# Performance work log

Hardware: AMD Instinct MI355X
Metric: run time of the kernel (lower is better)

Reference implementation:

```python
import jax, jax.numpy as jnp
import numpy as np

B = 16384
FEAT_SIZES = [1000000, 1000000, 500000, 500000, 100000, 100000, 10000, 10000]
EMB_DIM = 50          # min(50, feat_size//2) for all chosen sizes
CONT_IN = 64
D = 8 * EMB_DIM + 64  # 464 = total_embedding_size + 64
H1, H2 = 256, 128     # expert/cross hidden sizes
E, T = 4, 3           # num_experts, num_tasks


def setup_inputs() -> dict:
    key = jax.random.key(0)
    ks = iter(jax.random.split(key, 64))
    s = 0.02
    inp = {}
    inp["discrete_features"] = jax.random.randint(next(ks), (B, 8), 0, 10000)
    inp["continuous_features"] = jax.random.normal(next(ks), (B, CONT_IN), jnp.float32)
    for i, fs in enumerate(FEAT_SIZES):
        inp[f"emb{i}"] = jax.random.normal(next(ks), (fs, EMB_DIM), jnp.float32) * s
    inp["cont_W"] = jax.random.normal(next(ks), (CONT_IN, 64), jnp.float32) * s
    inp["cont_b"] = jnp.zeros((64,), jnp.float32)
    inp["fm_W"] = jax.random.normal(next(ks), (D, 10), jnp.float32) * s
    inp["cW1"] = jax.random.normal(next(ks), (D, H1), jnp.float32) * s
    inp["cb1"] = jnp.zeros((H1,), jnp.float32)
    inp["cW2"] = jax.random.normal(next(ks), (H1, H2), jnp.float32) * s
    inp["cb2"] = jnp.zeros((H2,), jnp.float32)
    inp["coW"] = jax.random.normal(next(ks), (H2, D), jnp.float32) * s
    inp["cob"] = jnp.zeros((D,), jnp.float32)
    inp["expW1"] = jax.random.normal(next(ks), (E, D, H1), jnp.float32) * s
    inp["expb1"] = jnp.zeros((E, H1), jnp.float32)
    inp["expW2"] = jax.random.normal(next(ks), (E, H1, H2), jnp.float32) * s
    inp["expb2"] = jnp.zeros((E, H2), jnp.float32)
    inp["gate_W"] = jax.random.normal(next(ks), (T, D, E), jnp.float32) * s
    inp["gate_b"] = jnp.zeros((T, E), jnp.float32)
    inp["task_W"] = jax.random.normal(next(ks), (T, H2, 1), jnp.float32) * s
    inp["task_b"] = jnp.zeros((T, 1), jnp.float32)
    inp["log_vars"] = jnp.zeros((T,), jnp.float32)
    return inp


def reference(discrete_features, continuous_features,
              emb0, emb1, emb2, emb3, emb4, emb5, emb6, emb7,
              cont_W, cont_b, fm_W, cW1, cb1, cW2, cb2, coW, cob,
              expW1, expb1, expW2, expb2, gate_W, gate_b,
              task_W, task_b, log_vars):
    tables = [emb0, emb1, emb2, emb3, emb4, emb5, emb6, emb7]
    embs = [jnp.take(t, discrete_features[:, i], axis=0) for i, t in enumerate(tables)]
    cont = jax.nn.relu(continuous_features @ cont_W + cont_b)           # [B,64]
    x = jnp.concatenate(embs + [cont], axis=1)                          # [B,D]
    # FM part: x @ fm_embedding.weight -> [B,10], square-of-sum minus sum-of-square
    xe = x @ fm_W
    fm = 0.5 * (jnp.sum(xe, 1, keepdims=True) ** 2
                - jnp.sum(xe ** 2, 1, keepdims=True))                   # [B,1]
    # cross network
    c = jax.nn.relu(x @ cW1 + cb1)
    c = jax.nn.relu(c @ cW2 + cb2)
    co = c @ coW + cob                                                  # [B,D]
    h = x + co + fm                                                     # [B,D] (fm broadcast)
    # experts as batched GEMMs: [B,E,H2]
    e1 = jax.nn.relu(jnp.einsum('bd,edh->beh', h, expW1) + expb1)
    eo = jnp.einsum('beh,eho->beo', e1, expW2) + expb2
    # gates: [B,T,E] softmax over experts
    g = jax.nn.softmax(jnp.einsum('bd,tde->bte', h, gate_W) + gate_b, axis=-1)
    mixed = jnp.einsum('bte,beo->bto', g, eo)                           # [B,T,H2]
    out = jnp.einsum('bto,tok->btk', mixed, task_W) + task_b            # [B,T,1]
    return out[..., 0], log_vars                                        # ([B,3], [3])
```

## Files before the change

### kernel.cpp

```cpp
#include <hip/hip_runtime.h>
#include <stdint.h>

typedef _Float16 f16;
typedef __attribute__((ext_vector_type(8))) _Float16 f16x8;
typedef __attribute__((ext_vector_type(4))) float    f32x4;

constexpr int BROWS = 16384;
constexpr int NTASK = 3;

constexpr int OFF_CW1 = 0;
constexpr int OFF_CW2 = OFF_CW1 + 256 * 480;
constexpr int OFF_COW = OFF_CW2 + 128 * 256;
constexpr int OFF_EW1 = OFF_COW + 512 * 128;
constexpr int OFF_EW2 = OFF_EW1 + 1024 * 480;
constexpr int OFF_FMW = OFF_EW2 + 512 * 256;
constexpr int OFF_GW  = OFF_FMW + 16 * 480;
constexpr int OFF_CTW = OFF_GW  + 16 * 480;
constexpr int PACK_TOTAL = OFF_CTW + 64 * 64;

__global__ __launch_bounds__(256)
void pack_all(const float* __restrict__ cW1, const float* __restrict__ cW2,
              const float* __restrict__ coW, const float* __restrict__ expW1,
              const float* __restrict__ expW2, const float* __restrict__ fmW,
              const float* __restrict__ gateW, const float* __restrict__ contW,
              f16* __restrict__ wp)
{
    const int idx = blockIdx.x * 256 + threadIdx.x;
    if (idx >= PACK_TOTAL) return;
    float v = 0.f;
    if (idx < OFF_CW2) {
        const int l = idx - OFF_CW1, n = l / 480, k = l % 480;
        if (k < 464) v = cW1[k * 256 + n];
    } else if (idx < OFF_COW) {
        const int l = idx - OFF_CW2, n = l / 256, k = l % 256;
        v = cW2[k * 128 + n];
    } else if (idx < OFF_EW1) {
        const int l = idx - OFF_COW, n = l / 128, k = l % 128;
        if (n < 464) v = coW[k * 464 + n];
    } else if (idx < OFF_EW2) {
        const int l = idx - OFF_EW1, n = l / 480, k = l % 480;
        const int e = n >> 8, nn = n & 255;
        if (k < 464) v = expW1[(e * 464 + k) * 256 + nn];
    } else if (idx < OFF_FMW) {
        const int l = idx - OFF_EW2, n = l / 256, k = l % 256;
        const int e = n >> 7, nn = n & 127;
        v = expW2[(e * 256 + k) * 128 + nn];
    } else if (idx < OFF_GW) {
        const int l = idx - OFF_FMW, c = l / 480, k = l % 480;
        if (c < 10 && k < 464) v = fmW[k * 10 + c];
    } else if (idx < OFF_CTW) {
        const int l = idx - OFF_GW, c = l / 480, k = l % 480;
        if (c < 12 && k < 464) {
            const int tt = c >> 2, e = c & 3;
            v = gateW[(tt * 464 + k) * 4 + e];
        }
    } else {
        const int l = idx - OFF_CTW, n = l / 64, k = l % 64;
        v = contW[k * 64 + n];
    }
    wp[idx] = (f16)v;
}

template<int MF, int NF, int KS, int LDA>
__device__ __forceinline__ void wave_gemm(
    const f16* __restrict__ As, int arow0,
    const f16* __restrict__ Bg, int bcol0, int ldb,
    f32x4 (&acc)[MF][NF], int lane)
{
    const int g = lane >> 4, rr = lane & 15;
#pragma unroll
    for (int kb = 0; kb < KS; ++kb) {
        const int ko = kb * 32 + g * 8;
        f16x8 bf[NF];
#pragma unroll
        for (int j = 0; j < NF; ++j)
            bf[j] = *(const f16x8*)(Bg + (long)(bcol0 + j * 16 + rr) * ldb + ko);
#pragma unroll
        for (int i = 0; i < MF; ++i) {
            const f16x8 af = *(const f16x8*)(As + (arow0 + i * 16 + rr) * LDA + ko);
#pragma unroll
            for (int j = 0; j < NF; ++j)
                acc[i][j] = __builtin_amdgcn_mfma_f32_16x16x32_f16(
                    af, bf[j], acc[i][j], 0, 0, 0);
        }
    }
}

__global__ __launch_bounds__(256, 1)
void mmoe_fused(const int* __restrict__ disc, const float* __restrict__ cf,
                const float* __restrict__ e0p, const float* __restrict__ e1p,
                const float* __restrict__ e2p, const float* __restrict__ e3p,
                const float* __restrict__ e4p, const float* __restrict__ e5p,
                const float* __restrict__ e6p, const float* __restrict__ e7p,
                const float* __restrict__ contB, const float* __restrict__ cb1,
                const float* __restrict__ cb2, const float* __restrict__ cob,
                const float* __restrict__ expb1, const float* __restrict__ expb2,
                const float* __restrict__ gateB, const float* __restrict__ taskW,
                const float* __restrict__ taskB, const float* __restrict__ logv,
                const f16* __restrict__ wp, float* __restrict__ out)
{
    __shared__ f16   sh_x [64][488];
    __shared__ f16   sh_c1[64][264];
    __shared__ f16   sh_c2[64][136];
    __shared__ float sh_g [64][12];
    __shared__ float sh_part[4][64][3];
    __shared__ float sh_fm[64];
    __shared__ const float* stabs[8];

    const int t = threadIdx.x;
    const int lane = t & 63, wave = t >> 6;
    const int g = lane >> 4, rr = lane & 15;
    const long r0 = (long)blockIdx.x * 64;

    const f16* cW1p = wp + OFF_CW1;
    const f16* cW2p = wp + OFF_CW2;
    const f16* coWp = wp + OFF_COW;
    const f16* eW1p = wp + OFF_EW1;
    const f16* eW2p = wp + OFF_EW2;
    const f16* fmWp = wp + OFF_FMW;
    const f16* gWp  = wp + OFF_GW;
    const f16* ctWp = wp + OFF_CTW;

    if (t == 0) {
        stabs[0] = e0p; stabs[1] = e1p; stabs[2] = e2p; stabs[3] = e3p;
        stabs[4] = e4p; stabs[5] = e5p; stabs[6] = e6p; stabs[7] = e7p;
    }
    __syncthreads();

    f16* cfp = (f16*)&sh_c2[0][0];
    for (int i = t; i < 64 * 24; i += 256) sh_x[i / 24][464 + i % 24] = (f16)0.f;
    for (int p = t; p < 512; p += 256) {
        const int r = p >> 3, tab = p & 7;
        const long fi = disc[(r0 + r) * 8 + tab];
        const float* src = stabs[tab] + fi * 50;
        f16* dst = &sh_x[r][tab * 50];
#pragma unroll
        for (int q = 0; q < 25; ++q) {
            const float2 v = *(const float2*)(src + q * 2);
            dst[q * 2] = (f16)v.x; dst[q * 2 + 1] = (f16)v.y;
        }
    }
    for (int i = t; i < 64 * 16; i += 256) {
        const int r = i >> 4, q = i & 15;
        const float4 v = *(const float4*)(cf + (r0 + r) * 64 + q * 4);
        f16* dst = cfp + r * 72 + q * 4;
        dst[0] = (f16)v.x; dst[1] = (f16)v.y; dst[2] = (f16)v.z; dst[3] = (f16)v.w;
    }
    __syncthreads();

    {
        f32x4 acc[4][1] = {};
        wave_gemm<4, 1, 2, 72>(cfp, 0, ctWp, wave * 16, 64, acc, lane);
        const int col = wave * 16 + rr;
        const float bv = contB[col];
#pragma unroll
        for (int i = 0; i < 4; ++i)
#pragma unroll
            for (int rx = 0; rx < 4; ++rx)
                sh_x[i * 16 + g * 4 + rx][400 + col] =
                    (f16)fmaxf(acc[i][0][rx] + bv, 0.f);
    }
    __syncthreads();

    {
        f32x4 a[1][1] = {};
        wave_gemm<1, 1, 15, 488>(&sh_x[0][0], wave * 16, fmWp, 0, 480, a, lane);
#pragma unroll
        for (int rx = 0; rx < 4; ++rx) {
            const float v = a[0][0][rx];
            float s = v, ss = v * v;
#pragma unroll
            for (int off = 1; off < 16; off <<= 1) {
                s += __shfl_xor(s, off, 64); ss += __shfl_xor(ss, off, 64);
            }
            if (rr == 0) sh_fm[wave * 16 + g * 4 + rx] = 0.5f * (s * s - ss);
        }
    }
    {
        f32x4 acc[4][4] = {};
        wave_gemm<4, 4, 15, 488>(&sh_x[0][0], 0, cW1p, wave * 64, 480, acc, lane);
#pragma unroll
        for (int j = 0; j < 4; ++j) {
            const int col = wave * 64 + j * 16 + rr;
            const float bv = cb1[col];
#pragma unroll
            for (int i = 0; i < 4; ++i)
#pragma unroll
                for (int rx = 0; rx < 4; ++rx)
                    sh_c1[i * 16 + g * 4 + rx][col] =
                        (f16)fmaxf(acc[i][j][rx] + bv, 0.f);
        }
    }
    __syncthreads();

    {
        f32x4 acc[4][2] = {};
        wave_gemm<4, 2, 8, 264>(&sh_c1[0][0], 0, cW2p, wave * 32, 256, acc, lane);
#pragma unroll
        for (int j = 0; j < 2; ++j) {
            const int col = wave * 32 + j * 16 + rr;
            const float bv = cb2[col];
#pragma unroll
            for (int i = 0; i < 4; ++i)
#pragma unroll
                for (int rx = 0; rx < 4; ++rx)
                    sh_c2[i * 16 + g * 4 + rx][col] =
                        (f16)fmaxf(acc[i][j][rx] + bv, 0.f);
        }
    }
    __syncthreads();

    {
        f32x4 acc[4][8] = {};
        wave_gemm<4, 8, 4, 136>(&sh_c2[0][0], 0, coWp, wave * 128, 128, acc, lane);
#pragma unroll
        for (int j = 0; j < 8; ++j) {
            const int col = wave * 128 + j * 16 + rr;
            if (col < 464) {
                const float bv = cob[col];
#pragma unroll
                for (int i = 0; i < 4; ++i)
#pragma unroll
                    for (int rx = 0; rx < 4; ++rx) {
                        const int row = i * 16 + g * 4 + rx;
                        const float v = acc[i][j][rx] + bv +
                                        (float)sh_x[row][col] + sh_fm[row];
                        sh_x[row][col] = (f16)v;
                    }
            }
        }
    }
    __syncthreads();

    {
        f32x4 a[1][1] = {};
        wave_gemm<1, 1, 15, 488>(&sh_x[0][0], wave * 16, gWp, 0, 480, a, lane);
        const float gb = (rr < 12) ? gateB[rr] : 0.f;
#pragma unroll
        for (int rx = 0; rx < 4; ++rx) {
            const float v = a[0][0][rx] + gb;
            float m = fmaxf(v, __shfl_xor(v, 1, 64));
            m = fmaxf(m, __shfl_xor(m, 2, 64));
            const float p = __expf(v - m);
            float s = p + __shfl_xor(p, 1, 64);
            s += __shfl_xor(s, 2, 64);
            if (rr < 12) sh_g[wave * 16 + g * 4 + rx][rr] = p / s;
        }
    }
    __syncthreads();

    float tw[3][2];
#pragma unroll
    for (int tt = 0; tt < 3; ++tt) {
        tw[tt][0] = taskW[tt * 128 + wave * 32 + rr];
        tw[tt][1] = taskW[tt * 128 + wave * 32 + 16 + rr];
    }
    float oacc[4][4][3];
#pragma unroll
    for (int i = 0; i < 4; ++i)
#pragma unroll
        for (int rx = 0; rx < 4; ++rx)
#pragma unroll
            for (int tt = 0; tt < 3; ++tt) oacc[i][rx][tt] = 0.f;

#pragma unroll 1
    for (int e = 0; e < 4; ++e) {
        {
            f32x4 acc[4][4] = {};
            wave_gemm<4, 4, 15, 488>(&sh_x[0][0], 0, eW1p + e * (256 * 480),
                                     wave * 64, 480, acc, lane);
#pragma unroll
            for (int j = 0; j < 4; ++j) {
                const int col = wave * 64 + j * 16 + rr;
                const float bv = expb1[e * 256 + col];
#pragma unroll
                for (int i = 0; i < 4; ++i)
#pragma unroll
                    for (int rx = 0; rx < 4; ++rx)
                        sh_c1[i * 16 + g * 4 + rx][col] =
                            (f16)fmaxf(acc[i][j][rx] + bv, 0.f);
            }
        }
        __syncthreads();
        {
            f32x4 acc[4][2] = {};
            wave_gemm<4, 2, 8, 264>(&sh_c1[0][0], 0, eW2p + e * (128 * 256),
                                    wave * 32, 256, acc, lane);
            const float bv0 = expb2[e * 128 + wave * 32 + rr];
            const float bv1 = expb2[e * 128 + wave * 32 + 16 + rr];
#pragma unroll
            for (int i = 0; i < 4; ++i)
#pragma unroll
                for (int rx = 0; rx < 4; ++rx) {
                    const int row = i * 16 + g * 4 + rx;
                    const float v0 = acc[i][0][rx] + bv0;
                    const float v1 = acc[i][1][rx] + bv1;
#pragma unroll
                    for (int tt = 0; tt < 3; ++tt) {
                        float s = v0 * tw[tt][0] + v1 * tw[tt][1];
#pragma unroll
                        for (int off = 1; off < 16; off <<= 1)
                            s += __shfl_xor(s, off, 64);
                        oacc[i][rx][tt] += sh_g[row][tt * 4 + e] * s;
                    }
                }
        }
        __syncthreads();
    }

    if (rr == 0) {
#pragma unroll
        for (int i = 0; i < 4; ++i)
#pragma unroll
            for (int rx = 0; rx < 4; ++rx)
#pragma unroll
                for (int tt = 0; tt < 3; ++tt)
                    sh_part[wave][i * 16 + g * 4 + rx][tt] = oacc[i][rx][tt];
    }
    __syncthreads();
    for (int i = t; i < 64 * 3; i += 256) {
        const int row = i / 3, tt = i - row * 3;
        out[(r0 + row) * 3 + tt] = sh_part[0][row][tt] + sh_part[1][row][tt] +
                                   sh_part[2][row][tt] + sh_part[3][row][tt] +
                                   taskB[tt];
    }
    if (blockIdx.x == 0 && t < NTASK) out[(long)BROWS * 3 + t] = logv[t];
}

extern "C" void kernel_launch(void* const* d_in, const int* in_sizes, int n_in,
                              void* d_out, int out_size, void* d_ws, size_t ws_size,
                              hipStream_t stream)
{
    (void)in_sizes; (void)n_in; (void)out_size; (void)ws_size;

    const int*   disc  = (const int*)  d_in[0];
    const float* cf    = (const float*)d_in[1];
    const float* emb0  = (const float*)d_in[2];
    const float* emb1  = (const float*)d_in[3];
    const float* emb2  = (const float*)d_in[4];
    const float* emb3  = (const float*)d_in[5];
    const float* emb4  = (const float*)d_in[6];
    const float* emb5  = (const float*)d_in[7];
    const float* emb6  = (const float*)d_in[8];
    const float* emb7  = (const float*)d_in[9];
    const float* contW = (const float*)d_in[10];
    const float* contB = (const float*)d_in[11];
    const float* fmW   = (const float*)d_in[12];
    const float* cW1   = (const float*)d_in[13];
    const float* cb1   = (const float*)d_in[14];
    const float* cW2   = (const float*)d_in[15];
    const float* cb2   = (const float*)d_in[16];
    const float* coW   = (const float*)d_in[17];
    const float* cob   = (const float*)d_in[18];
    const float* expW1 = (const float*)d_in[19];
    const float* expb1 = (const float*)d_in[20];
    const float* expW2 = (const float*)d_in[21];
    const float* expb2 = (const float*)d_in[22];
    const float* gateW = (const float*)d_in[23];
    const float* gateB = (const float*)d_in[24];
    const float* taskW = (const float*)d_in[25];
    const float* taskB = (const float*)d_in[26];
    const float* logv  = (const float*)d_in[27];

    f16* wp = (f16*)d_ws;

    pack_all<<<(PACK_TOTAL + 255) / 256, 256, 0, stream>>>(
        cW1, cW2, coW, expW1, expW2, fmW, gateW, contW, wp);

    mmoe_fused<<<BROWS / 64, 256, 0, stream>>>(
        disc, cf, emb0, emb1, emb2, emb3, emb4, emb5, emb6, emb7,
        contB, cb1, cb2, cob, expb1, expb2, gateB, taskW, taskB, logv,
        wp, (float*)d_out);
}
```

Before: 100.7 us.

## Use 512-thread blocks, split GEMM columns across 8 waves, defer task-head reduction

Doubles the workgroup to 8 waves, so each wave computes half as many output columns in every GEMM stage. This cuts per-wave accumulator registers and adds more waves to hide latency. The per-expert shuffle reduction for the task head is replaced by per-lane accumulation, with a single cross-lane reduction at the end. The fm and gate stages now use only 4 of the 8 waves, and A-fragment loads from shared memory are duplicated across more waves.

Measured after the change: 106.5 us. 1.06x slower.

```diff
diff --git a/kernel.cpp b/kernel.cpp
--- a/kernel.cpp
+++ b/kernel.cpp
@@ -86,7 +86,7 @@
     }
 }
 
-__global__ __launch_bounds__(256, 1)
+__global__ __launch_bounds__(512, 1)
 void mmoe_fused(const int* __restrict__ disc, const float* __restrict__ cf,
                 const float* __restrict__ e0p, const float* __restrict__ e1p,
                 const float* __restrict__ e2p, const float* __restrict__ e3p,
@@ -103,7 +103,7 @@
     __shared__ f16   sh_c1[64][264];
     __shared__ f16   sh_c2[64][136];
     __shared__ float sh_g [64][12];
-    __shared__ float sh_part[4][64][3];
+    __shared__ float sh_part[8][64][3];
     __shared__ float sh_fm[64];
     __shared__ const float* stabs[8];
 
@@ -128,9 +128,9 @@
     __syncthreads();
 
     f16* cfp = (f16*)&sh_c2[0][0];
-    for (int i = t; i < 64 * 24; i += 256) sh_x[i / 24][464 + i % 24] = (f16)0.f;
-    for (int p = t; p < 512; p += 256) {
-        const int r = p >> 3, tab = p & 7;
+    for (int i = t; i < 64 * 24; i += 512) sh_x[i / 24][464 + i % 24] = (f16)0.f;
+    {
+        const int r = t >> 3, tab = t & 7;
         const long fi = disc[(r0 + r) * 8 + tab];
         const float* src = stabs[tab] + fi * 50;
         f16* dst = &sh_x[r][tab * 50];
@@ -140,7 +140,7 @@
             dst[q * 2] = (f16)v.x; dst[q * 2 + 1] = (f16)v.y;
         }
     }
-    for (int i = t; i < 64 * 16; i += 256) {
+    for (int i = t; i < 64 * 16; i += 512) {
         const int r = i >> 4, q = i & 15;
         const float4 v = *(const float4*)(cf + (r0 + r) * 64 + q * 4);
         f16* dst = cfp + r * 72 + q * 4;
@@ -149,20 +149,21 @@
     __syncthreads();
 
     {
-        f32x4 acc[4][1] = {};
-        wave_gemm<4, 1, 2, 72>(cfp, 0, ctWp, wave * 16, 64, acc, lane);
-        const int col = wave * 16 + rr;
+        const int wm = wave >> 2, wn = wave & 3;
+        f32x4 acc[2][1] = {};
+        wave_gemm<2, 1, 2, 72>(cfp, wm * 32, ctWp, wn * 16, 64, acc, lane);
+        const int col = wn * 16 + rr;
         const float bv = contB[col];
 #pragma unroll
-        for (int i = 0; i < 4; ++i)
+        for (int i = 0; i < 2; ++i)
 #pragma unroll
             for (int rx = 0; rx < 4; ++rx)
-                sh_x[i * 16 + g * 4 + rx][400 + col] =
+                sh_x[wm * 32 + i * 16 + g * 4 + rx][400 + col] =
                     (f16)fmaxf(acc[i][0][rx] + bv, 0.f);
     }
     __syncthreads();
 
-    {
+    if (wave < 4) {
         f32x4 a[1][1] = {};
         wave_gemm<1, 1, 15, 488>(&sh_x[0][0], wave * 16, fmWp, 0, 480, a, lane);
 #pragma unroll
@@ -177,11 +178,11 @@
         }
     }
     {
-        f32x4 acc[4][4] = {};
-        wave_gemm<4, 4, 15, 488>(&sh_x[0][0], 0, cW1p, wave * 64, 480, acc, lane);
-#pragma unroll
-        for (int j = 0; j < 4; ++j) {
-            const int col = wave * 64 + j * 16 + rr;
+        f32x4 acc[4][2] = {};
+        wave_gemm<4, 2, 15, 488>(&sh_x[0][0], 0, cW1p, wave * 32, 480, acc, lane);
+#pragma unroll
+        for (int j = 0; j < 2; ++j) {
+            const int col = wave * 32 + j * 16 + rr;
             const float bv = cb1[col];
 #pragma unroll
             for (int i = 0; i < 4; ++i)
@@ -194,28 +195,25 @@
     __syncthreads();
 
     {
-        f32x4 acc[4][2] = {};
-        wave_gemm<4, 2, 8, 264>(&sh_c1[0][0], 0, cW2p, wave * 32, 256, acc, lane);
-#pragma unroll
-        for (int j = 0; j < 2; ++j) {
-            const int col = wave * 32 + j * 16 + rr;
-            const float bv = cb2[col];
-#pragma unroll
-            for (int i = 0; i < 4; ++i)
-#pragma unroll
-                for (int rx = 0; rx < 4; ++rx)
-                    sh_c2[i * 16 + g * 4 + rx][col] =
-                        (f16)fmaxf(acc[i][j][rx] + bv, 0.f);
-        }
-    }
-    __syncthreads();
-
-    {
-        f32x4 acc[4][8] = {};
-        wave_gemm<4, 8, 4, 136>(&sh_c2[0][0], 0, coWp, wave * 128, 128, acc, lane);
-#pragma unroll
-        for (int j = 0; j < 8; ++j) {
-            const int col = wave * 128 + j * 16 + rr;
+        f32x4 acc[4][1] = {};
+        wave_gemm<4, 1, 8, 264>(&sh_c1[0][0], 0, cW2p, wave * 16, 256, acc, lane);
+        const int col = wave * 16 + rr;
+        const float bv = cb2[col];
+#pragma unroll
+        for (int i = 0; i < 4; ++i)
+#pragma unroll
+            for (int rx = 0; rx < 4; ++rx)
+                sh_c2[i * 16 + g * 4 + rx][col] =
+                    (f16)fmaxf(acc[i][0][rx] + bv, 0.f);
+    }
+    __syncthreads();
+
+    {
+        f32x4 acc[4][4] = {};
+        wave_gemm<4, 4, 4, 136>(&sh_c2[0][0], 0, coWp, wave * 64, 128, acc, lane);
+#pragma unroll
+        for (int j = 0; j < 4; ++j) {
+            const int col = wave * 64 + j * 16 + rr;
             if (col < 464) {
                 const float bv = cob[col];
 #pragma unroll
@@ -232,7 +230,7 @@
     }
     __syncthreads();
 
-    {
+    if (wave < 4) {
         f32x4 a[1][1] = {};
         wave_gemm<1, 1, 15, 488>(&sh_x[0][0], wave * 16, gWp, 0, 480, a, lane);
         const float gb = (rr < 12) ? gateB[rr] : 0.f;
@@ -249,12 +247,10 @@
     }
     __syncthreads();
 
-    float tw[3][2];
-#pragma unroll
-    for (int tt = 0; tt < 3; ++tt) {
-        tw[tt][0] = taskW[tt * 128 + wave * 32 + rr];
-        tw[tt][1] = taskW[tt * 128 + wave * 32 + 16 + rr];
-    }
+    float tw[3];
+#pragma unroll
+    for (int tt = 0; tt < 3; ++tt) tw[tt] = taskW[tt * 128 + wave * 16 + rr];
+
     float oacc[4][4][3];
 #pragma unroll
     for (int i = 0; i < 4; ++i)
@@ -263,15 +259,15 @@
 #pragma unroll
             for (int tt = 0; tt < 3; ++tt) oacc[i][rx][tt] = 0.f;
 
-#pragma unroll 1
+#pragma unroll
     for (int e = 0; e < 4; ++e) {
         {
-            f32x4 acc[4][4] = {};
-            wave_gemm<4, 4, 15, 488>(&sh_x[0][0], 0, eW1p + e * (256 * 480),
-                                     wave * 64, 480, acc, lane);
-#pragma unroll
-            for (int j = 0; j < 4; ++j) {
-                const int col = wave * 64 + j * 16 + rr;
+            f32x4 acc[4][2] = {};
+            wave_gemm<4, 2, 15, 488>(&sh_x[0][0], 0, eW1p + e * (256 * 480),
+                                     wave * 32, 480, acc, lane);
+#pragma unroll
+            for (int j = 0; j < 2; ++j) {
+                const int col = wave * 32 + j * 16 + rr;
                 const float bv = expb1[e * 256 + col];
 #pragma unroll
                 for (int i = 0; i < 4; ++i)
@@ -283,46 +279,44 @@
         }
         __syncthreads();
         {
-            f32x4 acc[4][2] = {};
-            wave_gemm<4, 2, 8, 264>(&sh_c1[0][0], 0, eW2p + e * (128 * 256),
-                                    wave * 32, 256, acc, lane);
-            const float bv0 = expb2[e * 128 + wave * 32 + rr];
-            const float bv1 = expb2[e * 128 + wave * 32 + 16 + rr];
+            f32x4 acc[4][1] = {};
+            wave_gemm<4, 1, 8, 264>(&sh_c1[0][0], 0, eW2p + e * (128 * 256),
+                                    wave * 16, 256, acc, lane);
+            const float bv = expb2[e * 128 + wave * 16 + rr];
 #pragma unroll
             for (int i = 0; i < 4; ++i)
 #pragma unroll
                 for (int rx = 0; rx < 4; ++rx) {
                     const int row = i * 16 + g * 4 + rx;
-                    const float v0 = acc[i][0][rx] + bv0;
-                    const float v1 = acc[i][1][rx] + bv1;
-#pragma unroll
-                    for (int tt = 0; tt < 3; ++tt) {
-                        float s = v0 * tw[tt][0] + v1 * tw[tt][1];
-#pragma unroll
-                        for (int off = 1; off < 16; off <<= 1)
-                            s += __shfl_xor(s, off, 64);
-                        oacc[i][rx][tt] += sh_g[row][tt * 4 + e] * s;
-                    }
+                    const float v0 = acc[i][0][rx] + bv;
+#pragma unroll
+                    for (int tt = 0; tt < 3; ++tt)
+                        oacc[i][rx][tt] += sh_g[row][tt * 4 + e] * (v0 * tw[tt]);
                 }
         }
         __syncthreads();
     }
 
-    if (rr == 0) {
-#pragma unroll
-        for (int i = 0; i < 4; ++i)
-#pragma unroll
-            for (int rx = 0; rx < 4; ++rx)
-#pragma unroll
-                for (int tt = 0; tt < 3; ++tt)
-                    sh_part[wave][i * 16 + g * 4 + rx][tt] = oacc[i][rx][tt];
-    }
-    __syncthreads();
-    for (int i = t; i < 64 * 3; i += 256) {
-        const int row = i / 3, tt = i - row * 3;
-        out[(r0 + row) * 3 + tt] = sh_part[0][row][tt] + sh_part[1][row][tt] +
-                                   sh_part[2][row][tt] + sh_part[3][row][tt] +
-                                   taskB[tt];
+#pragma unroll
+    for (int i = 0; i < 4; ++i)
+#pragma unroll
+        for (int rx = 0; rx < 4; ++rx)
+#pragma unroll
+            for (int tt = 0; tt < 3; ++tt) {
+                float s = oacc[i][rx][tt];
+#pragma unroll
+                for (int off = 1; off < 16; off <<= 1)
+                    s += __shfl_xor(s, off, 64);
+                if (rr == 0)
+                    sh_part[wave][i * 16 + g * 4 + rx][tt] = s;
+            }
+    __syncthreads();
+    if (t < 64 * 3) {
+        const int row = t / 3, tt = t - row * 3;
+        float s = taskB[tt];
+#pragma unroll
+        for (int w = 0; w < 8; ++w) s += sh_part[w][row][tt];
+        out[(r0 + row) * 3 + tt] = s;
     }
     if (blockIdx.x == 0 && t < NTASK) out[(long)BROWS * 3 + t] = logv[t];
 }
@@ -367,7 +361,7 @@
     pack_all<<<(PACK_TOTAL + 255) / 256, 256, 0, stream>>>(
         cW1, cW2, coW, expW1, expW2, fmW, gateW, contW, wp);
 
-    mmoe_fused<<<BROWS / 64, 256, 0, stream>>>(
+    mmoe_fused<<<BROWS / 64, 512, 0, stream>>>(
         disc, cf, emb0, emb1, emb2, emb3, emb4, emb5, emb6, emb7,
         contB, cb1, cb2, cob, expb1, expb2, gateB, taskW, taskB, logv,
         wp, (float*)d_out);
```

## Halve rows per block to 32 and allow two blocks per CU

Applied to the files above, without the earlier changes.

Each block now processes 32 rows instead of 64, doubling the grid to 512 blocks and setting launch bounds to two blocks per CU. Shared memory and accumulator sizes shrink so more waves can be resident, which should improve latency hiding for the embedding gathers and weight loads. The task-head shuffle reduction moves out of the expert loop into a single final reduction, and the expert loop is fully unrolled. The FM and gate GEMMs now run on only two waves, and one barrier after the gate stage is removed, which relies on the barrier inside the expert loop to order the gate writes. The trade-off is that the weight matrices are reread from cache twice as often per row.

Result: slower. 107.0 us (+6.2%).

```diff
diff --git a/kernel.cpp b/kernel.cpp
--- a/kernel.cpp
+++ b/kernel.cpp
@@ -6,7 +6,7 @@
 typedef __attribute__((ext_vector_type(4))) float    f32x4;
 
 constexpr int BROWS = 16384;
-constexpr int NTASK = 3;
+constexpr int ROWS  = 32;
 
 constexpr int OFF_CW1 = 0;
 constexpr int OFF_CW2 = OFF_CW1 + 256 * 480;
@@ -86,7 +86,7 @@
     }
 }
 
-__global__ __launch_bounds__(256, 1)
+__global__ __launch_bounds__(256, 2)
 void mmoe_fused(const int* __restrict__ disc, const float* __restrict__ cf,
                 const float* __restrict__ e0p, const float* __restrict__ e1p,
                 const float* __restrict__ e2p, const float* __restrict__ e3p,
@@ -99,18 +99,18 @@
                 const float* __restrict__ taskB, const float* __restrict__ logv,
                 const f16* __restrict__ wp, float* __restrict__ out)
 {
-    __shared__ f16   sh_x [64][488];
-    __shared__ f16   sh_c1[64][264];
-    __shared__ f16   sh_c2[64][136];
-    __shared__ float sh_g [64][12];
-    __shared__ float sh_part[4][64][3];
-    __shared__ float sh_fm[64];
+    __shared__ f16   sh_x [ROWS][488];
+    __shared__ f16   sh_c1[ROWS][264];
+    __shared__ f16   sh_c2[ROWS][136];
+    __shared__ float sh_g [ROWS][12];
+    __shared__ float sh_part[4][ROWS][3];
+    __shared__ float sh_fm[ROWS];
     __shared__ const float* stabs[8];
 
     const int t = threadIdx.x;
     const int lane = t & 63, wave = t >> 6;
     const int g = lane >> 4, rr = lane & 15;
-    const long r0 = (long)blockIdx.x * 64;
+    const long r0 = (long)blockIdx.x * ROWS;
 
     const f16* cW1p = wp + OFF_CW1;
     const f16* cW2p = wp + OFF_CW2;
@@ -128,9 +128,9 @@
     __syncthreads();
 
     f16* cfp = (f16*)&sh_c2[0][0];
-    for (int i = t; i < 64 * 24; i += 256) sh_x[i / 24][464 + i % 24] = (f16)0.f;
-    for (int p = t; p < 512; p += 256) {
-        const int r = p >> 3, tab = p & 7;
+    for (int i = t; i < ROWS * 24; i += 256) sh_x[i / 24][464 + i % 24] = (f16)0.f;
+    {
+        const int r = t >> 3, tab = t & 7;
         const long fi = disc[(r0 + r) * 8 + tab];
         const float* src = stabs[tab] + fi * 50;
         f16* dst = &sh_x[r][tab * 50];
@@ -140,7 +140,7 @@
             dst[q * 2] = (f16)v.x; dst[q * 2 + 1] = (f16)v.y;
         }
     }
-    for (int i = t; i < 64 * 16; i += 256) {
+    for (int i = t; i < ROWS * 16; i += 256) {
         const int r = i >> 4, q = i & 15;
         const float4 v = *(const float4*)(cf + (r0 + r) * 64 + q * 4);
         f16* dst = cfp + r * 72 + q * 4;
@@ -149,12 +149,12 @@
     __syncthreads();
 
     {
-        f32x4 acc[4][1] = {};
-        wave_gemm<4, 1, 2, 72>(cfp, 0, ctWp, wave * 16, 64, acc, lane);
+        f32x4 acc[2][1] = {};
+        wave_gemm<2, 1, 2, 72>(cfp, 0, ctWp, wave * 16, 64, acc, lane);
         const int col = wave * 16 + rr;
         const float bv = contB[col];
 #pragma unroll
-        for (int i = 0; i < 4; ++i)
+        for (int i = 0; i < 2; ++i)
 #pragma unroll
             for (int rx = 0; rx < 4; ++rx)
                 sh_x[i * 16 + g * 4 + rx][400 + col] =
@@ -162,7 +162,7 @@
     }
     __syncthreads();
 
-    {
+    if (wave < 2) {
         f32x4 a[1][1] = {};
         wave_gemm<1, 1, 15, 488>(&sh_x[0][0], wave * 16, fmWp, 0, 480, a, lane);
 #pragma unroll
@@ -177,14 +177,14 @@
         }
     }
     {
-        f32x4 acc[4][4] = {};
-        wave_gemm<4, 4, 15, 488>(&sh_x[0][0], 0, cW1p, wave * 64, 480, acc, lane);
+        f32x4 acc[2][4] = {};
+        wave_gemm<2, 4, 15, 488>(&sh_x[0][0], 0, cW1p, wave * 64, 480, acc, lane);
 #pragma unroll
         for (int j = 0; j < 4; ++j) {
             const int col = wave * 64 + j * 16 + rr;
             const float bv = cb1[col];
 #pragma unroll
-            for (int i = 0; i < 4; ++i)
+            for (int i = 0; i < 2; ++i)
 #pragma unroll
                 for (int rx = 0; rx < 4; ++rx)
                     sh_c1[i * 16 + g * 4 + rx][col] =
@@ -194,14 +194,14 @@
     __syncthreads();
 
     {
-        f32x4 acc[4][2] = {};
-        wave_gemm<4, 2, 8, 264>(&sh_c1[0][0], 0, cW2p, wave * 32, 256, acc, lane);
+        f32x4 acc[2][2] = {};
+        wave_gemm<2, 2, 8, 264>(&sh_c1[0][0], 0, cW2p, wave * 32, 256, acc, lane);
 #pragma unroll
         for (int j = 0; j < 2; ++j) {
             const int col = wave * 32 + j * 16 + rr;
             const float bv = cb2[col];
 #pragma unroll
-            for (int i = 0; i < 4; ++i)
+            for (int i = 0; i < 2; ++i)
 #pragma unroll
                 for (int rx = 0; rx < 4; ++rx)
                     sh_c2[i * 16 + g * 4 + rx][col] =
@@ -211,15 +211,15 @@
     __syncthreads();
 
     {
-        f32x4 acc[4][8] = {};
-        wave_gemm<4, 8, 4, 136>(&sh_c2[0][0], 0, coWp, wave * 128, 128, acc, lane);
+        f32x4 acc[2][8] = {};
+        wave_gemm<2, 8, 4, 136>(&sh_c2[0][0], 0, coWp, wave * 128, 128, acc, lane);
 #pragma unroll
         for (int j = 0; j < 8; ++j) {
             const int col = wave * 128 + j * 16 + rr;
             if (col < 464) {
                 const float bv = cob[col];
 #pragma unroll
-                for (int i = 0; i < 4; ++i)
+                for (int i = 0; i < 2; ++i)
 #pragma unroll
                     for (int rx = 0; rx < 4; ++rx) {
                         const int row = i * 16 + g * 4 + rx;
@@ -232,7 +232,7 @@
     }
     __syncthreads();
 
-    {
+    if (wave < 2) {
         f32x4 a[1][1] = {};
         wave_gemm<1, 1, 15, 488>(&sh_x[0][0], wave * 16, gWp, 0, 480, a, lane);
         const float gb = (rr < 12) ? gateB[rr] : 0.f;
@@ -247,7 +247,6 @@
             if (rr < 12) sh_g[wave * 16 + g * 4 + rx][rr] = p / s;
         }
     }
-    __syncthreads();
 
     float tw[3][2];
 #pragma unroll
@@ -255,26 +254,26 @@
         tw[tt][0] = taskW[tt * 128 + wave * 32 + rr];
         tw[tt][1] = taskW[tt * 128 + wave * 32 + 16 + rr];
     }
-    float oacc[4][4][3];
-#pragma unroll
-    for (int i = 0; i < 4; ++i)
+    float oacc[2][4][3];
+#pragma unroll
+    for (int i = 0; i < 2; ++i)
 #pragma unroll
         for (int rx = 0; rx < 4; ++rx)
 #pragma unroll
             for (int tt = 0; tt < 3; ++tt) oacc[i][rx][tt] = 0.f;
 
-#pragma unroll 1
+#pragma unroll
     for (int e = 0; e < 4; ++e) {
         {
-            f32x4 acc[4][4] = {};
-            wave_gemm<4, 4, 15, 488>(&sh_x[0][0], 0, eW1p + e * (256 * 480),
-                                     wave * 64, 480, acc, lane);
+            f32x4 acc[2][4] = {};
+            wave_gemm<2, 4, 15, 488>(&sh_x[0][0], 0, eW1p, e * 256 + wave * 64, 480,
+                                     acc, lane);
 #pragma unroll
             for (int j = 0; j < 4; ++j) {
                 const int col = wave * 64 + j * 16 + rr;
                 const float bv = expb1[e * 256 + col];
 #pragma unroll
-                for (int i = 0; i < 4; ++i)
+                for (int i = 0; i < 2; ++i)
 #pragma unroll
                     for (int rx = 0; rx < 4; ++rx)
                         sh_c1[i * 16 + g * 4 + rx][col] =
@@ -283,48 +282,49 @@
         }
         __syncthreads();
         {
-            f32x4 acc[4][2] = {};
-            wave_gemm<4, 2, 8, 264>(&sh_c1[0][0], 0, eW2p + e * (128 * 256),
-                                    wave * 32, 256, acc, lane);
+            f32x4 acc[2][2] = {};
+            wave_gemm<2, 2, 8, 264>(&sh_c1[0][0], 0, eW2p, e * 128 + wave * 32, 256,
+                                    acc, lane);
             const float bv0 = expb2[e * 128 + wave * 32 + rr];
             const float bv1 = expb2[e * 128 + wave * 32 + 16 + rr];
 #pragma unroll
-            for (int i = 0; i < 4; ++i)
+            for (int i = 0; i < 2; ++i)
 #pragma unroll
                 for (int rx = 0; rx < 4; ++rx) {
                     const int row = i * 16 + g * 4 + rx;
                     const float v0 = acc[i][0][rx] + bv0;
                     const float v1 = acc[i][1][rx] + bv1;
 #pragma unroll
-                    for (int tt = 0; tt < 3; ++tt) {
-                        float s = v0 * tw[tt][0] + v1 * tw[tt][1];
-#pragma unroll
-                        for (int off = 1; off < 16; off <<= 1)
-                            s += __shfl_xor(s, off, 64);
-                        oacc[i][rx][tt] += sh_g[row][tt * 4 + e] * s;
-                    }
+                    for (int tt = 0; tt < 3; ++tt)
+                        oacc[i][rx][tt] += sh_g[row][tt * 4 + e] *
+                                           (v0 * tw[tt][0] + v1 * tw[tt][1]);
                 }
         }
         __syncthreads();
     }
 
-    if (rr == 0) {
-#pragma unroll
-        for (int i = 0; i < 4; ++i)
-#pragma unroll
-            for (int rx = 0; rx < 4; ++rx)
-#pragma unroll
-                for (int tt = 0; tt < 3; ++tt)
-                    sh_part[wave][i * 16 + g * 4 + rx][tt] = oacc[i][rx][tt];
-    }
-    __syncthreads();
-    for (int i = t; i < 64 * 3; i += 256) {
-        const int row = i / 3, tt = i - row * 3;
-        out[(r0 + row) * 3 + tt] = sh_part[0][row][tt] + sh_part[1][row][tt] +
-                                   sh_part[2][row][tt] + sh_part[3][row][tt] +
-                                   taskB[tt];
-    }
-    if (blockIdx.x == 0 && t < NTASK) out[(long)BROWS * 3 + t] = logv[t];
+#pragma unroll
+    for (int i = 0; i < 2; ++i)
+#pragma unroll
+        for (int rx = 0; rx < 4; ++rx)
+#pragma unroll
+            for (int tt = 0; tt < 3; ++tt) {
+                float s = oacc[i][rx][tt];
+#pragma unroll
+                for (int off = 1; off < 16; off <<= 1)
+                    s += __shfl_xor(s, off, 64);
+                if (rr == 0)
+                    sh_part[wave][i * 16 + g * 4 + rx][tt] = s;
+            }
+    __syncthreads();
+    if (t < ROWS * 3) {
+        const int row = t / 3, tt = t - row * 3;
+        float s = taskB[tt];
+#pragma unroll
+        for (int w = 0; w < 4; ++w) s += sh_part[w][row][tt];
+        out[(r0 + row) * 3 + tt] = s;
+    }
+    if (blockIdx.x == 0 && t < 3) out[(long)BROWS * 3 + t] = logv[t];
 }
 
 extern "C" void kernel_launch(void* const* d_in, const int* in_sizes, int n_in,
@@ -367,7 +367,7 @@
     pack_all<<<(PACK_TOTAL + 255) / 256, 256, 0, stream>>>(
         cW1, cW2, coW, expW1, expW2, fmW, gateW, contW, wp);
 
-    mmoe_fused<<<BROWS / 64, 256, 0, stream>>>(
+    mmoe_fused<<<BROWS / ROWS, 256, 0, stream>>>(
         disc, cf, emb0, emb1, emb2, emb3, emb4, emb5, emb6, emb7,
         contB, cb1, cb2, cob, expb1, expb2, gateB, taskW, taskB, logv,
         wp, (float*)d_out);
```
